# Kernel tuning notes

Hardware: AMD Instinct MI355X
Metric: run time of the kernel (lower is better)

Reference implementation:

```python
import jax, jax.numpy as jnp
import numpy as np

B = 8192
D = 1024
NUM_CLASSES = 128
EPS = 1e-8  # torch F.cosine_similarity default eps


def setup_inputs() -> dict:
    key = jax.random.key(0)
    k1, k2, k3 = jax.random.split(key, 3)
    label_tensor = jax.random.randint(k1, (B,), 0, NUM_CLASSES, dtype=jnp.int64 if jax.config.jax_enable_x64 else jnp.int32)
    feature_a = jax.random.normal(k2, (B, D), dtype=jnp.float32)
    feature_b = jax.random.normal(k3, (B, D), dtype=jnp.float32)
    return {"label_tensor": label_tensor, "feature_a": feature_a, "feature_b": feature_b}


def reference(label_tensor, feature_a, feature_b):
    # Pairwise cosine similarity: cos_score[i, k] = cos(a_i, b_k), shape [B, B]
    dots = feature_a @ feature_b.T  # [B, B]
    na = jnp.linalg.norm(feature_a, axis=1)  # [B]
    nb = jnp.linalg.norm(feature_b, axis=1)  # [B]
    cos_score = dots / jnp.maximum(na[:, None] * nb[None, :], EPS)
    # Row-softmax (torch softmax dim=1 on the [B, B] matrix)
    logp = jax.nn.log_softmax(cos_score, axis=1)
    # Label-equality mask: positives for row i are all j with same label
    mask = (label_tensor[:, None] == label_tensor[None, :]).astype(cos_score.dtype)  # [B, B]
    per_row = -(mask * logp).sum(axis=1) / mask.sum(axis=1)  # diagonal guarantees >=1 positive
    loss = per_row.mean()
    return loss, cos_score
```

## Files before the change

kernel.cpp:

```cpp
#include <hip/hip_runtime.h>
#include <hip/hip_bf16.h>

#define NB 8192
#define ND 1024

typedef int   i32x4 __attribute__((ext_vector_type(4)));
typedef int   i32x8 __attribute__((ext_vector_type(8)));
typedef float f32x4 __attribute__((ext_vector_type(4)));

__device__ inline void gload_lds16(const void* g, void* l) {
    __builtin_amdgcn_global_load_lds(
        (const __attribute__((address_space(1))) unsigned int*)g,
        (__attribute__((address_space(3))) unsigned int*)l,
        16, 0, 0);
}

#define BARRIER() asm volatile("s_barrier" ::: "memory")
#define VMCNT0()  asm volatile("s_waitcnt vmcnt(0)" ::: "memory")
#define VMCNT8()  asm volatile("s_waitcnt vmcnt(8)" ::: "memory")

__global__ __launch_bounds__(256) void prep_kernel(
    const float* __restrict__ A, const float* __restrict__ Bm,
    unsigned char* __restrict__ wa, unsigned char* __restrict__ wb,
    float* __restrict__ na, float* __restrict__ nb)
{
    int b = blockIdx.x;
    int wid = threadIdx.x >> 6, lane = threadIdx.x & 63;
    const float* src; unsigned char* dst; float* nrm; int row;
    if (b < 2048) { src = A;  dst = wa; nrm = na; row = b * 4 + wid; }
    else          { src = Bm; dst = wb; nrm = nb; row = (b - 2048) * 4 + wid; }

    const float*   rp = src + (size_t)row * ND;
    unsigned char* wp = dst + (size_t)row * ND;

    float ss = 0.f;
#pragma unroll
    for (int t = 0; t < 4; ++t) {
        int c = lane * 4 + t * 256;
        float4 v = *reinterpret_cast<const float4*>(rp + c);
        ss += v.x * v.x + v.y * v.y + v.z * v.z + v.w * v.w;
        int u = __builtin_amdgcn_cvt_pk_fp8_f32(v.x, v.y, 0, false);
        u     = __builtin_amdgcn_cvt_pk_fp8_f32(v.z, v.w, u, true);
        *reinterpret_cast<unsigned int*>(wp + c) = (unsigned int)u;
    }
#pragma unroll
    for (int off = 32; off; off >>= 1) ss += __shfl_xor(ss, off);
    if (lane == 0) nrm[row] = sqrtf(ss);
}

__global__ __launch_bounds__(256) void hist_kernel(
    const int* __restrict__ labels, int* __restrict__ hist)
{
    __shared__ int h[128];
    int tid = threadIdx.x;
    if (tid < 128) h[tid] = 0;
    __syncthreads();
    for (int i = tid; i < NB; i += 256) atomicAdd(&h[labels[i]], 1);
    __syncthreads();
    if (tid < 128) hist[tid] = h[tid];
}

__global__ __launch_bounds__(256) void gemm_cos(
    const unsigned char* __restrict__ wa, const unsigned char* __restrict__ wb,
    const float* __restrict__ na, const float* __restrict__ nb,
    const int* __restrict__ labels,
    float* __restrict__ C, float* __restrict__ pe, float* __restrict__ pm)
{
    __shared__ __align__(16) unsigned char lds8[65536];

    const int bid = blockIdx.x;
    const int swz = (bid & 7) * 512 + (bid >> 3);
    const int tm  = swz >> 6, tn = swz & 63;

    const int tid  = threadIdx.x;
    const int lane = tid & 63;
    const int wid  = tid >> 6;
    const int wr   = wid >> 1, wc = wid & 1;
    const int l15  = lane & 15, lg = lane >> 4;

    const int m0 = tm * 128, n0 = tn * 128;

    const int srow = tid >> 3;
    const int sgr  = (tid & 7) ^ (srow & 7);
    const unsigned char* pA = wa + (size_t)(m0 + srow) * ND + sgr * 16;
    const unsigned char* pB = wb + (size_t)(n0 + srow) * ND + sgr * 16;
    const int stW = wid * 1024;

    const int gsw  = (((2 * lg) ^ (l15 & 7)) * 16);
    const int aoff = (wr * 64 + l15) * 128 + gsw;
    const int boff = 16384 + (wc * 64 + l15) * 128 + gsw;

    f32x4 acc[4][4];
#pragma unroll
    for (int i = 0; i < 4; ++i)
#pragma unroll
        for (int j = 0; j < 4; ++j) acc[i][j] = (f32x4){0.f, 0.f, 0.f, 0.f};

#define STAGE(kt, BUF) do { \
    _Pragma("unroll") \
    for (int i_ = 0; i_ < 4; ++i_) { \
        gload_lds16(pA + (size_t)i_ * 32 * ND + (kt) * 128, \
                    &lds8[(BUF) + i_ * 4096 + stW]); \
        gload_lds16(pB + (size_t)i_ * 32 * ND + (kt) * 128, \
                    &lds8[(BUF) + 16384 + i_ * 4096 + stW]); \
    } } while (0)

#define RD32(off) __builtin_shufflevector( \
    *reinterpret_cast<const i32x4*>(&lds8[(off)]), \
    *reinterpret_cast<const i32x4*>(&lds8[(off) ^ 16]), 0, 1, 2, 3, 4, 5, 6, 7)

    STAGE(0, 0);
#pragma unroll
    for (int kt = 0; kt < 8; ++kt) {
        const int cb = (kt & 1) * 32768;
        if (kt < 7) { STAGE(kt + 1, cb ^ 32768); VMCNT8(); }
        else        { VMCNT0(); }
        BARRIER();
        i32x8 bq[4];
#pragma unroll
        for (int n = 0; n < 4; ++n) bq[n] = RD32(cb + boff + n * 2048);
#pragma unroll
        for (int m = 0; m < 4; ++m) {
            i32x8 am = RD32(cb + aoff + m * 2048);
#pragma unroll
            for (int n = 0; n < 4; ++n)
                acc[m][n] = __builtin_amdgcn_mfma_scale_f32_16x16x128_f8f6f4(
                    am, bq[n], acc[m][n], 0, 0, 0, 127, 0, 127);
        }
        BARRIER();
    }

#undef RD32
#undef STAGE

    __syncthreads();
    float* pl = reinterpret_cast<float*>(lds8);

    float nbv[4]; int labc[4];
#pragma unroll
    for (int n = 0; n < 4; ++n) {
        int c = n0 + wc * 64 + n * 16 + l15;
        nbv[n] = nb[c]; labc[n] = labels[c];
    }

#pragma unroll
    for (int m = 0; m < 4; ++m) {
#pragma unroll
        for (int jj = 0; jj < 4; ++jj) {
            int rl = wr * 64 + m * 16 + lg * 4 + jj;
            int r  = m0 + rl;
            float nav = na[r]; int labr = labels[r];
            float es = 0.f, ms = 0.f;
#pragma unroll
            for (int n = 0; n < 4; ++n) {
                int c = n0 + wc * 64 + n * 16 + l15;
                float v = acc[m][n][jj] / fmaxf(nav * nbv[n], 1e-8f);
                __builtin_nontemporal_store(v, &C[(size_t)r * NB + c]);
                es += __expf(v);
                ms += (labc[n] == labr) ? v : 0.f;
            }
#pragma unroll
            for (int off = 1; off < 16; off <<= 1) {
                es += __shfl_xor(es, off);
                ms += __shfl_xor(ms, off);
            }
            if (l15 == 0) {
                int o = rl * 4 + wc * 2;
                pl[o] = es; pl[o + 1] = ms;
            }
        }
    }
    __syncthreads();
    if (tid < 128) {
        float es = pl[tid * 4]     + pl[tid * 4 + 2];
        float ms = pl[tid * 4 + 1] + pl[tid * 4 + 3];
        pe[tn * NB + m0 + tid] = es;
        pm[tn * NB + m0 + tid] = ms;
    }
}

__global__ __launch_bounds__(256) void loss_final(
    const float* __restrict__ pe, const float* __restrict__ pm,
    const int* __restrict__ labels, const int* __restrict__ hist,
    float* __restrict__ per_row)
{
    int row = blockIdx.x * 256 + threadIdx.x;
    float es = 0.f, ms = 0.f;
#pragma unroll
    for (int t = 0; t < 64; ++t) {
        es += pe[t * NB + row];
        ms += pm[t * NB + row];
    }
    per_row[row] = logf(es) - ms / (float)hist[labels[row]];
}

__global__ __launch_bounds__(256) void finalize(
    const float* __restrict__ per_row, float* __restrict__ out)
{
    __shared__ float sm[256];
    float s = 0.f;
    for (int i = threadIdx.x; i < NB; i += 256) s += per_row[i];
    sm[threadIdx.x] = s;
    __syncthreads();
    for (int k = 128; k; k >>= 1) {
        if (threadIdx.x < k) sm[threadIdx.x] += sm[threadIdx.x + k];
        __syncthreads();
    }
    if (threadIdx.x == 0) out[0] = sm[0] * (1.0f / (float)NB);
}

extern "C" void kernel_launch(void* const* d_in, const int* in_sizes, int n_in,
                              void* d_out, int out_size, void* d_ws, size_t ws_size,
                              hipStream_t stream) {
    const int*   labels = (const int*)d_in[0];
    const float* A      = (const float*)d_in[1];
    const float* Bm     = (const float*)d_in[2];
    float* out = (float*)d_out;

    char* ws = (char*)d_ws;
    unsigned char* wa = (unsigned char*)(ws);
    unsigned char* wb = (unsigned char*)(ws + 8388608);
    float* na      = (float*)(ws + 16777216);
    float* nb      = (float*)(ws + 16809984);
    float* per_row = (float*)(ws + 16842752);
    int*   hist    = (int*)  (ws + 16875520);
    float* pe      = (float*)(ws + 16908288);
    float* pm      = (float*)(ws + 19005440);

    float* cosm = out + 1;

    prep_kernel<<<4096, 256, 0, stream>>>(A, Bm, wa, wb, na, nb);
    hist_kernel<<<1,    256, 0, stream>>>(labels, hist);
    gemm_cos   <<<4096, 256, 0, stream>>>(wa, wb, na, nb, labels, cosm, pe, pm);
    loss_final <<<32,   256, 0, stream>>>(pe, pm, labels, hist, per_row);
    finalize   <<<1,    256, 0, stream>>>(per_row, out);
}
```

Before: 278.9 us.

## Pre-tile FP8 operands into MFMA-ready layout and restructure GEMM pipeline

The prep kernel now writes FP8 operands in a tiled, MFMA-fragment-ordered layout, one 128-row panel per tile. This lets the GEMM stage each K-tile with fully contiguous 16-byte loads and read LDS without XOR swizzling. The main loop now issues the next stage before computing and waits for all loads at the end of each iteration. Block-to-tile mapping changes to a different swizzle, and the nontemporal stores for the cosine matrix become plain stores. Risks include LDS bank conflicts from the unswizzled reads, less overlap from the full vmcnt(0) wait, and altered L2/cache behaviour for the large output.

```diff
diff --git a/kernel.cpp b/kernel.cpp
--- a/kernel.cpp
+++ b/kernel.cpp
@@ -17,21 +17,22 @@
 
 #define BARRIER() asm volatile("s_barrier" ::: "memory")
 #define VMCNT0()  asm volatile("s_waitcnt vmcnt(0)" ::: "memory")
-#define VMCNT8()  asm volatile("s_waitcnt vmcnt(8)" ::: "memory")
+#define LGKM0()   asm volatile("s_waitcnt lgkmcnt(0)" ::: "memory")
 
 __global__ __launch_bounds__(256) void prep_kernel(
     const float* __restrict__ A, const float* __restrict__ Bm,
-    unsigned char* __restrict__ wa, unsigned char* __restrict__ wb,
+    unsigned char* __restrict__ wa2, unsigned char* __restrict__ wb2,
     float* __restrict__ na, float* __restrict__ nb)
 {
     int b = blockIdx.x;
     int wid = threadIdx.x >> 6, lane = threadIdx.x & 63;
-    const float* src; unsigned char* dst; float* nrm; int row;
-    if (b < 2048) { src = A;  dst = wa; nrm = na; row = b * 4 + wid; }
-    else          { src = Bm; dst = wb; nrm = nb; row = (b - 2048) * 4 + wid; }
-
-    const float*   rp = src + (size_t)row * ND;
-    unsigned char* wp = dst + (size_t)row * ND;
+    bool isA = (b < 2048);
+    int row = (isA ? b : b - 2048) * 4 + wid;
+    const float*   rp  = (isA ? A : Bm) + (size_t)row * ND;
+    unsigned char* dst = (isA ? wa2 : wb2);
+
+    const size_t pbase = (size_t)(row >> 7) * 131072 + ((row >> 4) & 7) * 2048;
+    const int    r15   = row & 15;
 
     float ss = 0.f;
 #pragma unroll
@@ -41,11 +42,13 @@
         ss += v.x * v.x + v.y * v.y + v.z * v.z + v.w * v.w;
         int u = __builtin_amdgcn_cvt_pk_fp8_f32(v.x, v.y, 0, false);
         u     = __builtin_amdgcn_cvt_pk_fp8_f32(v.z, v.w, u, true);
-        *reinterpret_cast<unsigned int*>(wp + c) = (unsigned int)u;
+        size_t addr = pbase + (size_t)(c >> 7) * 16384 + ((c >> 4) & 1) * 1024
+                    + (((c >> 5) & 3) * 16 + r15) * 16 + (c & 15);
+        *reinterpret_cast<unsigned int*>(dst + addr) = (unsigned int)u;
     }
 #pragma unroll
     for (int off = 32; off; off >>= 1) ss += __shfl_xor(ss, off);
-    if (lane == 0) nrm[row] = sqrtf(ss);
+    if (lane == 0) (isA ? na : nb)[row] = sqrtf(ss);
 }
 
 __global__ __launch_bounds__(256) void hist_kernel(
@@ -61,7 +64,7 @@
 }
 
 __global__ __launch_bounds__(256) void gemm_cos(
-    const unsigned char* __restrict__ wa, const unsigned char* __restrict__ wb,
+    const unsigned char* __restrict__ wa2, const unsigned char* __restrict__ wb2,
     const float* __restrict__ na, const float* __restrict__ nb,
     const int* __restrict__ labels,
     float* __restrict__ C, float* __restrict__ pe, float* __restrict__ pm)
@@ -69,8 +72,8 @@
     __shared__ __align__(16) unsigned char lds8[65536];
 
     const int bid = blockIdx.x;
-    const int swz = (bid & 7) * 512 + (bid >> 3);
-    const int tm  = swz >> 6, tn = swz & 63;
+    const int tm  = (bid & 7) * 8 + ((bid >> 3) & 7);
+    const int tn  = bid >> 6;
 
     const int tid  = threadIdx.x;
     const int lane = tid & 63;
@@ -80,15 +83,12 @@
 
     const int m0 = tm * 128, n0 = tn * 128;
 
-    const int srow = tid >> 3;
-    const int sgr  = (tid & 7) ^ (srow & 7);
-    const unsigned char* pA = wa + (size_t)(m0 + srow) * ND + sgr * 16;
-    const unsigned char* pB = wb + (size_t)(n0 + srow) * ND + sgr * 16;
+    const unsigned char* pA = wa2 + (size_t)tm * 131072 + tid * 16;
+    const unsigned char* pB = wb2 + (size_t)tn * 131072 + tid * 16;
     const int stW = wid * 1024;
 
-    const int gsw  = (((2 * lg) ^ (l15 & 7)) * 16);
-    const int aoff = (wr * 64 + l15) * 128 + gsw;
-    const int boff = 16384 + (wc * 64 + l15) * 128 + gsw;
+    const int afb = wr * 8192 + lane * 16;
+    const int bqb = 16384 + wc * 8192 + lane * 16;
 
     f32x4 acc[4][4];
 #pragma unroll
@@ -99,37 +99,45 @@
 #define STAGE(kt, BUF) do { \
     _Pragma("unroll") \
     for (int i_ = 0; i_ < 4; ++i_) { \
-        gload_lds16(pA + (size_t)i_ * 32 * ND + (kt) * 128, \
+        gload_lds16(pA + (kt) * 16384 + i_ * 4096, \
                     &lds8[(BUF) + i_ * 4096 + stW]); \
-        gload_lds16(pB + (size_t)i_ * 32 * ND + (kt) * 128, \
+        gload_lds16(pB + (kt) * 16384 + i_ * 4096, \
                     &lds8[(BUF) + 16384 + i_ * 4096 + stW]); \
     } } while (0)
 
 #define RD32(off) __builtin_shufflevector( \
     *reinterpret_cast<const i32x4*>(&lds8[(off)]), \
-    *reinterpret_cast<const i32x4*>(&lds8[(off) ^ 16]), 0, 1, 2, 3, 4, 5, 6, 7)
+    *reinterpret_cast<const i32x4*>(&lds8[(off) + 1024]), 0, 1, 2, 3, 4, 5, 6, 7)
+
+#define COMPUTE(BUF) do { \
+    i32x8 bq[4]; \
+    _Pragma("unroll") \
+    for (int n_ = 0; n_ < 4; ++n_) bq[n_] = RD32((BUF) + bqb + n_ * 2048); \
+    _Pragma("unroll") \
+    for (int m_ = 0; m_ < 4; ++m_) { \
+        i32x8 am = RD32((BUF) + afb + m_ * 2048); \
+        _Pragma("unroll") \
+        for (int n_ = 0; n_ < 4; ++n_) \
+            acc[m_][n_] = __builtin_amdgcn_mfma_scale_f32_16x16x128_f8f6f4( \
+                am, bq[n_], acc[m_][n_], 0, 0, 0, 127, 0, 127); \
+    } } while (0)
 
     STAGE(0, 0);
-#pragma unroll
-    for (int kt = 0; kt < 8; ++kt) {
-        const int cb = (kt & 1) * 32768;
-        if (kt < 7) { STAGE(kt + 1, cb ^ 32768); VMCNT8(); }
-        else        { VMCNT0(); }
+    VMCNT0();
+    BARRIER();
+
+#pragma unroll
+    for (int t = 0; t < 8; ++t) {
+        const int cb = (t & 1) * 32768;
+        if (t < 7) STAGE(t + 1, cb ^ 32768);
+        COMPUTE(cb);
+        __builtin_amdgcn_sched_barrier(0);
+        VMCNT0();
+        LGKM0();
         BARRIER();
-        i32x8 bq[4];
-#pragma unroll
-        for (int n = 0; n < 4; ++n) bq[n] = RD32(cb + boff + n * 2048);
-#pragma unroll
-        for (int m = 0; m < 4; ++m) {
-            i32x8 am = RD32(cb + aoff + m * 2048);
-#pragma unroll
-            for (int n = 0; n < 4; ++n)
-                acc[m][n] = __builtin_amdgcn_mfma_scale_f32_16x16x128_f8f6f4(
-                    am, bq[n], acc[m][n], 0, 0, 0, 127, 0, 127);
-        }
-        BARRIER();
-    }
-
+    }
+
+#undef COMPUTE
 #undef RD32
 #undef STAGE
 
@@ -155,7 +163,7 @@
             for (int n = 0; n < 4; ++n) {
                 int c = n0 + wc * 64 + n * 16 + l15;
                 float v = acc[m][n][jj] / fmaxf(nav * nbv[n], 1e-8f);
-                __builtin_nontemporal_store(v, &C[(size_t)r * NB + c]);
+                C[(size_t)r * NB + c] = v;
                 es += __expf(v);
                 ms += (labc[n] == labr) ? v : 0.f;
             }
@@ -218,8 +226,8 @@
     float* out = (float*)d_out;
 
     char* ws = (char*)d_ws;
-    unsigned char* wa = (unsigned char*)(ws);
-    unsigned char* wb = (unsigned char*)(ws + 8388608);
+    unsigned char* wa2 = (unsigned char*)(ws);
+    unsigned char* wb2 = (unsigned char*)(ws + 8388608);
     float* na      = (float*)(ws + 16777216);
     float* nb      = (float*)(ws + 16809984);
     float* per_row = (float*)(ws + 16842752);
@@ -229,9 +237,9 @@
 
     float* cosm = out + 1;
 
-    prep_kernel<<<4096, 256, 0, stream>>>(A, Bm, wa, wb, na, nb);
+    prep_kernel<<<4096, 256, 0, stream>>>(A, Bm, wa2, wb2, na, nb);
     hist_kernel<<<1,    256, 0, stream>>>(labels, hist);
-    gemm_cos   <<<4096, 256, 0, stream>>>(wa, wb, na, nb, labels, cosm, pe, pm);
+    gemm_cos   <<<4096, 256, 0, stream>>>(wa2, wb2, na, nb, labels, cosm, pe, pm);
     loss_final <<<32,   256, 0, stream>>>(pe, pm, labels, hist, per_row);
     finalize   <<<1,    256, 0, stream>>>(per_row, out);
 }
```

Result: slower. 292.8 us (+5.0%).
